# Performance work log

Measured on AMD Instinct MI355X. Metric: run time of the kernel, lower is better.

The kernel has to match this reference:

```python
import jax, jax.numpy as jnp
import numpy as np

N_NODES = 100000
N_EDGES = 1600000
N_GRAPHS = 512


def gcn_conv(x, W, b, src, dst, n_nodes):
    """GCNConv with self-loops: D^-1/2 (A+I) D^-1/2 X W + b."""
    h = x @ W  # [N, out]
    ones = jnp.ones((src.shape[0],), h.dtype)
    deg = jax.ops.segment_sum(ones, dst, num_segments=n_nodes) + 1.0  # +1 self-loop
    dinv = jax.lax.rsqrt(deg)
    norm = dinv[src] * dinv[dst]  # [E]
    agg = jax.ops.segment_sum(h[src] * norm[:, None], dst, num_segments=n_nodes)
    agg = agg + h * (1.0 / deg)[:, None]  # self-loop term: deg^-0.5 * deg^-0.5
    return agg + b


def setup_inputs() -> dict:
    key = jax.random.key(0)
    ks = jax.random.split(key, 12)
    x = jax.random.normal(ks[0], (N_NODES, 78), dtype=jnp.float32)
    edge_index = jax.random.randint(ks[1], (2, N_EDGES), 0, N_NODES, dtype=jnp.int64)
    batch = jnp.sort(jax.random.randint(ks[2], (N_NODES,), 0, N_GRAPHS, dtype=jnp.int64))
    def glorot(k, shape):
        lim = np.sqrt(6.0 / (shape[0] + shape[1])).astype(np.float32)
        return jax.random.uniform(k, shape, jnp.float32, -lim, lim)
    return {
        "x": x,
        "edge_index": edge_index,
        "batch": batch,
        "W1": glorot(ks[3], (78, 128)),
        "b1": jnp.zeros((128,), jnp.float32),
        "W2": glorot(ks[4], (128, 256)),
        "b2": jnp.zeros((256,), jnp.float32),
        "Wg1": glorot(ks[5], (256, 1024)),
        "bg1": jnp.zeros((1024,), jnp.float32),
        "Wg2": glorot(ks[6], (1024, 128)),
        "bg2": jnp.zeros((128,), jnp.float32),
    }


def reference(x, edge_index, batch, W1, b1, W2, b2, Wg1, bg1, Wg2, bg2):
    src, dst = edge_index[0], edge_index[1]
    n = x.shape[0]
    h = jax.nn.relu(gcn_conv(x, W1, b1, src, dst, n))   # [N,128]
    h = jax.nn.relu(gcn_conv(h, W2, b2, src, dst, n))   # [N,256]
    g = jax.ops.segment_max(h, batch, num_segments=N_GRAPHS)  # global max pool [G,256]
    g = jax.nn.relu(g @ Wg1 + bg1)   # [G,1024]; dropout is identity at eval
    g = g @ Wg2 + bg2                # [G,128]
    return g
```

## Files before the change

### kernel.cpp

```cpp
#include <hip/hip_runtime.h>
#include <hip/hip_bf16.h>


#define NN 100000
#define NE 1600000
#define NG 512
#define NBLK ((NN + 1023) / 1024)

typedef float v2f __attribute__((ext_vector_type(2)));


__global__ void k_zero_int(int* p, int n) {
    int i = blockIdx.x * blockDim.x + threadIdx.x;
    if (i < n) p[i] = 0;
}

__global__ void k_hist(const int* __restrict__ dst, int* cnt, int e) {
    int i = blockIdx.x * blockDim.x + threadIdx.x;
    if (i < e) atomicAdd(&cnt[dst[i]], 1);
}

__global__ void k_prep(const int* __restrict__ cnt, float* __restrict__ dinv,
                       float* __restrict__ gmax) {
    int i = blockIdx.x * blockDim.x + threadIdx.x;
    if (i < NN) dinv[i] = rsqrtf((float)cnt[i] + 1.0f);
    if (i < NG * 256) gmax[i] = 0.0f;
}

__global__ __launch_bounds__(256) void k_bsum(const int* __restrict__ cnt, int* __restrict__ bsum) {
    __shared__ int s[256];
    int b = blockIdx.x, t = threadIdx.x;
    int base = b * 1024 + t * 4;
    int v = 0;
#pragma unroll
    for (int j = 0; j < 4; j++) { int i = base + j; if (i < NN) v += cnt[i]; }
    s[t] = v; __syncthreads();
    for (int off = 128; off > 0; off >>= 1) {
        if (t < off) s[t] += s[t + off];
        __syncthreads();
    }
    if (t == 0) bsum[b] = s[0];
}

__global__ __launch_bounds__(128) void k_scan_bsum(int* bsum, int* row_ptr) {
    __shared__ int s[128];
    int t = threadIdx.x;
    int v = (t < NBLK) ? bsum[t] : 0;
    s[t] = v; __syncthreads();
    for (int off = 1; off < 128; off <<= 1) {
        int u = (t >= off) ? s[t - off] : 0;
        __syncthreads();
        s[t] += u;
        __syncthreads();
    }
    if (t < NBLK) bsum[t] = s[t] - v;
    if (t == 0) row_ptr[NN] = NE;
}

__global__ __launch_bounds__(256) void k_scan_blocks(const int* __restrict__ cnt,
    const int* __restrict__ bsum, int* __restrict__ row_ptr, int* __restrict__ cursor) {
    __shared__ int s[256];
    int b = blockIdx.x, t = threadIdx.x;
    int base = b * 1024 + t * 4;
    int v[4]; int sum = 0;
#pragma unroll
    for (int j = 0; j < 4; j++) { int i = base + j; v[j] = (i < NN) ? cnt[i] : 0; sum += v[j]; }
    s[t] = sum; __syncthreads();
    for (int off = 1; off < 256; off <<= 1) {
        int u = (t >= off) ? s[t - off] : 0;
        __syncthreads();
        s[t] += u;
        __syncthreads();
    }
    int excl = s[t] - sum + bsum[b];
#pragma unroll
    for (int j = 0; j < 4; j++) {
        int i = base + j;
        if (i < NN) { row_ptr[i] = excl; cursor[i] = excl; excl += v[j]; }
    }
}

__global__ void k_fillslots(const int* __restrict__ src, const int* __restrict__ dst,
    const float* __restrict__ dinv, int* cursor, int2* __restrict__ es, int e) {
    int i = blockIdx.x * blockDim.x + threadIdx.x;
    if (i >= e) return;
    int s = src[i], d = dst[i];
    int pos = atomicAdd(&cursor[d], 1);
    es[pos] = make_int2(s, __float_as_int(dinv[s] * dinv[d]));
}

__global__ __launch_bounds__(256) void k_fused1(const float* __restrict__ x,
    const int* __restrict__ rp, const int2* __restrict__ es,
    const float* __restrict__ dinv, const float* __restrict__ W,
    const float* __restrict__ bias, float* __restrict__ out) {
    __shared__ float As[4][8][80];
    int tid = threadIdx.x;
    int wv = tid >> 6, l = tid & 63;
    int task = __builtin_amdgcn_readfirstlane(blockIdx.x * 4 + wv);
    int n0 = task * 8;
    if (n0 >= NN) return;

    if (l < 39) {
        for (int pi = 0; pi < 4; pi++) {
            int nA = n0 + 2 * pi, nB = nA + 1;
            float diA = dinv[nA], swA = diA * diA;
            float diB = dinv[nB], swB = diB * diB;
            float2 aA = ((const float2*)(x + (size_t)nA * 78))[l];
            float2 aB = ((const float2*)(x + (size_t)nB * 78))[l];
            aA.x *= swA; aA.y *= swA;
            aB.x *= swB; aB.y *= swB;
            int eA = rp[nA], eA1 = rp[nA + 1];
            int eB = rp[nB], eB1 = rp[nB + 1];
            int cA = (eA1 - eA) >> 3, cB = (eB1 - eB) >> 3;
            while (cA > 0 || cB > 0) {
                bool dA = (cA > 0), dB = (cB > 0);
                int2 esA[8], esB[8];
                float2 vA[8], vB[8];
                if (dA) {
#pragma unroll
                    for (int j = 0; j < 8; j++) esA[j] = es[eA + j];
                }
                if (dB) {
#pragma unroll
                    for (int j = 0; j < 8; j++) esB[j] = es[eB + j];
                }
                if (dA) {
#pragma unroll
                    for (int j = 0; j < 8; j++)
                        vA[j] = ((const float2*)(x + (size_t)esA[j].x * 78))[l];
                }
                if (dB) {
#pragma unroll
                    for (int j = 0; j < 8; j++)
                        vB[j] = ((const float2*)(x + (size_t)esB[j].x * 78))[l];
                }
                if (dA) {
#pragma unroll
                    for (int j = 0; j < 8; j++) {
                        float w = __int_as_float(esA[j].y);
                        aA.x += vA[j].x * w; aA.y += vA[j].y * w;
                    }
                    eA += 8; cA--;
                }
                if (dB) {
#pragma unroll
                    for (int j = 0; j < 8; j++) {
                        float w = __int_as_float(esB[j].y);
                        aB.x += vB[j].x * w; aB.y += vB[j].y * w;
                    }
                    eB += 8; cB--;
                }
            }
            while (eA < eA1 && eB < eB1) {
                int2 pA = es[eA], pB = es[eB];
                float2 vA2 = ((const float2*)(x + (size_t)pA.x * 78))[l];
                float2 vB2 = ((const float2*)(x + (size_t)pB.x * 78))[l];
                float wA = __int_as_float(pA.y), wB = __int_as_float(pB.y);
                aA.x += vA2.x * wA; aA.y += vA2.y * wA;
                aB.x += vB2.x * wB; aB.y += vB2.y * wB;
                eA++; eB++;
            }
            for (; eA < eA1; eA++) {
                int2 p = es[eA];
                float w = __int_as_float(p.y);
                float2 v = ((const float2*)(x + (size_t)p.x * 78))[l];
                aA.x += v.x * w; aA.y += v.y * w;
            }
            for (; eB < eB1; eB++) {
                int2 p = es[eB];
                float w = __int_as_float(p.y);
                float2 v = ((const float2*)(x + (size_t)p.x * 78))[l];
                aB.x += v.x * w; aB.y += v.y * w;
            }
            *(float2*)&As[wv][2 * pi][2 * l] = aA;
            *(float2*)&As[wv][2 * pi + 1][2 * l] = aB;
        }
    }

    int f0 = l * 2;
    float2 acc[8];
#pragma unroll
    for (int i = 0; i < 8; i++) acc[i] = make_float2(0.f, 0.f);

    for (int k = 0; k < 76; k += 4) {
        float2 w0 = *(const float2*)&W[(k + 0) * 128 + f0];
        float2 w1 = *(const float2*)&W[(k + 1) * 128 + f0];
        float2 w2 = *(const float2*)&W[(k + 2) * 128 + f0];
        float2 w3 = *(const float2*)&W[(k + 3) * 128 + f0];
#pragma unroll
        for (int i = 0; i < 8; i++) {
            float4 a = *(const float4*)&As[wv][i][k];
            acc[i].x += a.x * w0.x + a.y * w1.x + a.z * w2.x + a.w * w3.x;
            acc[i].y += a.x * w0.y + a.y * w1.y + a.z * w2.y + a.w * w3.y;
        }
    }
    {
        float2 w0 = *(const float2*)&W[76 * 128 + f0];
        float2 w1 = *(const float2*)&W[77 * 128 + f0];
#pragma unroll
        for (int i = 0; i < 8; i++) {
            float2 a = *(const float2*)&As[wv][i][76];
            acc[i].x += a.x * w0.x + a.y * w1.x;
            acc[i].y += a.x * w0.y + a.y * w1.y;
        }
    }
    float2 bv = *(const float2*)&bias[f0];
#pragma unroll
    for (int i = 0; i < 8; i++) {
        float2 o;
        o.x = fmaxf(acc[i].x + bv.x, 0.f);
        o.y = fmaxf(acc[i].y + bv.y, 0.f);
        *(float2*)&out[(size_t)(n0 + i) * 128 + f0] = o;
    }
}

__global__ __launch_bounds__(256) void k_fused2(const float* __restrict__ h,
    const int* __restrict__ rp, const int2* __restrict__ es,
    const float* __restrict__ dinv, const float* __restrict__ W,
    const float* __restrict__ bias, const int* __restrict__ batch,
    unsigned* __restrict__ gmax) {
    __shared__ float As[4][8][128];
    int tid = threadIdx.x;
    int wv = tid >> 6, l = tid & 63;
    int task = __builtin_amdgcn_readfirstlane(blockIdx.x * 4 + wv);
    int n0 = task * 8;
    if (n0 >= NN) return;

    for (int pi = 0; pi < 4; pi++) {
        int nA = n0 + 2 * pi, nB = nA + 1;
        float diA = dinv[nA], swA = diA * diA;
        float diB = dinv[nB], swB = diB * diB;
        float2 aA = ((const float2*)(h + (size_t)nA * 128))[l];
        float2 aB = ((const float2*)(h + (size_t)nB * 128))[l];
        aA.x *= swA; aA.y *= swA;
        aB.x *= swB; aB.y *= swB;
        int eA = rp[nA], eA1 = rp[nA + 1];
        int eB = rp[nB], eB1 = rp[nB + 1];
        int cA = (eA1 - eA) >> 3, cB = (eB1 - eB) >> 3;
        while (cA > 0 || cB > 0) {
            bool dA = (cA > 0), dB = (cB > 0);
            int2 esA[8], esB[8];
            float2 vA[8], vB[8];
            if (dA) {
#pragma unroll
                for (int j = 0; j < 8; j++) esA[j] = es[eA + j];
            }
            if (dB) {
#pragma unroll
                for (int j = 0; j < 8; j++) esB[j] = es[eB + j];
            }
            if (dA) {
#pragma unroll
                for (int j = 0; j < 8; j++)
                    vA[j] = ((const float2*)(h + (size_t)esA[j].x * 128))[l];
            }
            if (dB) {
#pragma unroll
                for (int j = 0; j < 8; j++)
                    vB[j] = ((const float2*)(h + (size_t)esB[j].x * 128))[l];
            }
            if (dA) {
#pragma unroll
                for (int j = 0; j < 8; j++) {
                    float w = __int_as_float(esA[j].y);
                    aA.x += vA[j].x * w; aA.y += vA[j].y * w;
                }
                eA += 8; cA--;
            }
            if (dB) {
#pragma unroll
                for (int j = 0; j < 8; j++) {
                    float w = __int_as_float(esB[j].y);
                    aB.x += vB[j].x * w; aB.y += vB[j].y * w;
                }
                eB += 8; cB--;
            }
        }
        while (eA < eA1 && eB < eB1) {
            int2 pA = es[eA], pB = es[eB];
            float2 vA2 = ((const float2*)(h + (size_t)pA.x * 128))[l];
            float2 vB2 = ((const float2*)(h + (size_t)pB.x * 128))[l];
            float wA = __int_as_float(pA.y), wB = __int_as_float(pB.y);
            aA.x += vA2.x * wA; aA.y += vA2.y * wA;
            aB.x += vB2.x * wB; aB.y += vB2.y * wB;
            eA++; eB++;
        }
        for (; eA < eA1; eA++) {
            int2 p = es[eA];
            float w = __int_as_float(p.y);
            float2 v = ((const float2*)(h + (size_t)p.x * 128))[l];
            aA.x += v.x * w; aA.y += v.y * w;
        }
        for (; eB < eB1; eB++) {
            int2 p = es[eB];
            float w = __int_as_float(p.y);
            float2 v = ((const float2*)(h + (size_t)p.x * 128))[l];
            aB.x += v.x * w; aB.y += v.y * w;
        }
        *(float2*)&As[wv][2 * pi][2 * l] = aA;
        *(float2*)&As[wv][2 * pi + 1][2 * l] = aB;
    }

    int f0 = l * 4;
    v2f acc[8][2];
#pragma unroll
    for (int i = 0; i < 8; i++) { acc[i][0] = (v2f)(0.f); acc[i][1] = (v2f)(0.f); }

    for (int k = 0; k < 128; k += 4) {
        float4 w0 = *(const float4*)&W[(size_t)(k + 0) * 256 + f0];
        float4 w1 = *(const float4*)&W[(size_t)(k + 1) * 256 + f0];
        float4 w2 = *(const float4*)&W[(size_t)(k + 2) * 256 + f0];
        float4 w3 = *(const float4*)&W[(size_t)(k + 3) * 256 + f0];
        v2f w0a = {w0.x, w0.y}, w0b = {w0.z, w0.w};
        v2f w1a = {w1.x, w1.y}, w1b = {w1.z, w1.w};
        v2f w2a = {w2.x, w2.y}, w2b = {w2.z, w2.w};
        v2f w3a = {w3.x, w3.y}, w3b = {w3.z, w3.w};
#pragma unroll
        for (int i = 0; i < 8; i++) {
            float4 a = *(const float4*)&As[wv][i][k];
            v2f sx = {a.x, a.x}, sy = {a.y, a.y}, sz = {a.z, a.z}, sw = {a.w, a.w};
            acc[i][0] = __builtin_elementwise_fma(sx, w0a, acc[i][0]);
            acc[i][1] = __builtin_elementwise_fma(sx, w0b, acc[i][1]);
            acc[i][0] = __builtin_elementwise_fma(sy, w1a, acc[i][0]);
            acc[i][1] = __builtin_elementwise_fma(sy, w1b, acc[i][1]);
            acc[i][0] = __builtin_elementwise_fma(sz, w2a, acc[i][0]);
            acc[i][1] = __builtin_elementwise_fma(sz, w2b, acc[i][1]);
            acc[i][0] = __builtin_elementwise_fma(sw, w3a, acc[i][0]);
            acc[i][1] = __builtin_elementwise_fma(sw, w3b, acc[i][1]);
        }
    }

    float4 bv = *(const float4*)&bias[f0];
    int curg = -1;
    float4 m = make_float4(0.f, 0.f, 0.f, 0.f);
#pragma unroll
    for (int i = 0; i < 8; i++) {
        int g = batch[n0 + i];
        float4 v;
        v.x = fmaxf(acc[i][0].x + bv.x, 0.f); v.y = fmaxf(acc[i][0].y + bv.y, 0.f);
        v.z = fmaxf(acc[i][1].x + bv.z, 0.f); v.w = fmaxf(acc[i][1].y + bv.w, 0.f);
        if (g != curg) {
            if (curg >= 0) {
                unsigned* gp = &gmax[(size_t)curg * 256 + f0];
                atomicMax(&gp[0], __float_as_uint(m.x));
                atomicMax(&gp[1], __float_as_uint(m.y));
                atomicMax(&gp[2], __float_as_uint(m.z));
                atomicMax(&gp[3], __float_as_uint(m.w));
            }
            curg = g; m = v;
        } else {
            m.x = fmaxf(m.x, v.x); m.y = fmaxf(m.y, v.y);
            m.z = fmaxf(m.z, v.z); m.w = fmaxf(m.w, v.w);
        }
    }
    if (curg >= 0) {
        unsigned* gp = &gmax[(size_t)curg * 256 + f0];
        atomicMax(&gp[0], __float_as_uint(m.x));
        atomicMax(&gp[1], __float_as_uint(m.y));
        atomicMax(&gp[2], __float_as_uint(m.z));
        atomicMax(&gp[3], __float_as_uint(m.w));
    }
}


__global__ __launch_bounds__(256) void k_gemm3(const float* __restrict__ A,
    const float* __restrict__ W, const float* __restrict__ bias,
    float* __restrict__ out) {
    __shared__ float rs[256];
    int g = blockIdx.x, tid = threadIdx.x;
    rs[tid] = A[g * 256 + tid];
    __syncthreads();
    float acc[4] = {0.f, 0.f, 0.f, 0.f};
    for (int k = 0; k < 256; k++) {
        float a = rs[k];
#pragma unroll
        for (int j = 0; j < 4; j++) acc[j] += a * W[k * 1024 + tid + j * 256];
    }
#pragma unroll
    for (int j = 0; j < 4; j++) {
        int f = tid + j * 256;
        out[g * 1024 + f] = fmaxf(acc[j] + bias[f], 0.0f);
    }
}

__global__ __launch_bounds__(128) void k_gemm4(const float* __restrict__ A,
    const float* __restrict__ W, const float* __restrict__ bias,
    float* __restrict__ out) {
    __shared__ float rs[1024];
    int g = blockIdx.x, tid = threadIdx.x;
    for (int i = tid; i < 1024; i += 128) rs[i] = A[g * 1024 + i];
    __syncthreads();
    float acc = 0.0f;
    for (int k = 0; k < 1024; k++) acc += rs[k] * W[k * 128 + tid];
    out[g * 128 + tid] = acc + bias[tid];
}

extern "C" void kernel_launch(void* const* d_in, const int* in_sizes, int n_in,
                              void* d_out, int out_size, void* d_ws, size_t ws_size,
                              hipStream_t stream) {
    const float* x    = (const float*)d_in[0];
    const int*   ei   = (const int*)d_in[1];
    const int*   batch= (const int*)d_in[2];
    const float* W1   = (const float*)d_in[3];
    const float* b1   = (const float*)d_in[4];
    const float* W2   = (const float*)d_in[5];
    const float* b2   = (const float*)d_in[6];
    const float* Wg1  = (const float*)d_in[7];
    const float* bg1  = (const float*)d_in[8];
    const float* Wg2  = (const float*)d_in[9];
    const float* bg2  = (const float*)d_in[10];
    const int* src = ei;
    const int* dst = ei + NE;

    char* w8 = (char*)d_ws;
    int*   cnt     = (int*)w8;                 w8 += (size_t)NN * 4;
    int*   row_ptr = (int*)w8;                 w8 += (size_t)(NN + 4) * 4;
    int*   cursor  = (int*)w8;                 w8 += (size_t)NN * 4;
    int*   bsum    = (int*)w8;                 w8 += 128 * 4;
    int2*  es      = (int2*)w8;                w8 += (size_t)NE * 8;
    float* dinv    = (float*)w8;               w8 += (size_t)NN * 4;
    float* h1      = (float*)w8;               w8 += (size_t)NN * 128 * 4;
    unsigned* gmax = (unsigned*)w8;            w8 += (size_t)NG * 256 * 4;
    float* g1      = (float*)w8;               w8 += (size_t)NG * 1024 * 4;

    k_zero_int<<<(NN + 255) / 256, 256, 0, stream>>>(cnt, NN);
    k_hist<<<(NE + 255) / 256, 256, 0, stream>>>(dst, cnt, NE);
    k_prep<<<(NG * 256 + 255) / 256, 256, 0, stream>>>(cnt, dinv, (float*)gmax);
    k_bsum<<<NBLK, 256, 0, stream>>>(cnt, bsum);
    k_scan_bsum<<<1, 128, 0, stream>>>(bsum, row_ptr);
    k_scan_blocks<<<NBLK, 256, 0, stream>>>(cnt, bsum, row_ptr, cursor);
    k_fillslots<<<(NE + 255) / 256, 256, 0, stream>>>(src, dst, dinv, cursor, es, NE);

    k_fused1<<<NN / 32, 256, 0, stream>>>(x, row_ptr, es, dinv, W1, b1, h1);

    k_fused2<<<NN / 32, 256, 0, stream>>>(h1, row_ptr, es, dinv, W2, b2, batch, gmax);

    k_gemm3<<<NG, 256, 0, stream>>>((const float*)gmax, Wg1, bg1, g1);
    k_gemm4<<<NG, 128, 0, stream>>>(g1, Wg2, bg2, (float*)d_out);
}
```

Baseline: 587.5 us.

## Process two node tiles per wave, batch four graphs in head GEMMs, memset counts

Result: slower. 911.0 us (+55.1%).

```diff
diff --git a/kernel.cpp b/kernel.cpp
--- a/kernel.cpp
+++ b/kernel.cpp
@@ -9,11 +9,6 @@
 
 typedef float v2f __attribute__((ext_vector_type(2)));
 
-
-__global__ void k_zero_int(int* p, int n) {
-    int i = blockIdx.x * blockDim.x + threadIdx.x;
-    if (i < n) p[i] = 0;
-}
 
 __global__ void k_hist(const int* __restrict__ dst, int* cnt, int e) {
     int i = blockIdx.x * blockDim.x + threadIdx.x;
@@ -96,17 +91,166 @@
     __shared__ float As[4][8][80];
     int tid = threadIdx.x;
     int wv = tid >> 6, l = tid & 63;
-    int task = __builtin_amdgcn_readfirstlane(blockIdx.x * 4 + wv);
-    int n0 = task * 8;
-    if (n0 >= NN) return;
-
+    int w = __builtin_amdgcn_readfirstlane(blockIdx.x * 4 + wv);
+    if (w >= 6250) return;
+    int n0 = w * 16;
+
+    int f0 = l * 2;
+    float2 bv = *(const float2*)&bias[f0];
+
+    float2 init[8];
     if (l < 39) {
+#pragma unroll
+        for (int i = 0; i < 8; i++)
+            init[i] = ((const float2*)(x + (size_t)(n0 + i) * 78))[l];
+    }
+
+    for (int it = 0; it < 2; it++) {
+        int b0 = n0 + it * 8;
+        if (l < 39) {
+            for (int pi = 0; pi < 4; pi++) {
+                int nA = b0 + 2 * pi, nB = nA + 1;
+                float diA = dinv[nA], swA = diA * diA;
+                float diB = dinv[nB], swB = diB * diB;
+                float2 aA = init[2 * pi], aB = init[2 * pi + 1];
+                aA.x *= swA; aA.y *= swA;
+                aB.x *= swB; aB.y *= swB;
+                int eA = rp[nA], eA1 = rp[nA + 1];
+                int eB = rp[nB], eB1 = rp[nB + 1];
+                int cA = (eA1 - eA) >> 3, cB = (eB1 - eB) >> 3;
+                while (cA > 0 || cB > 0) {
+                    bool dA = (cA > 0), dB = (cB > 0);
+                    int2 esA[8], esB[8];
+                    float2 vA[8], vB[8];
+                    if (dA) {
+#pragma unroll
+                        for (int j = 0; j < 8; j++) esA[j] = es[eA + j];
+                    }
+                    if (dB) {
+#pragma unroll
+                        for (int j = 0; j < 8; j++) esB[j] = es[eB + j];
+                    }
+                    if (dA) {
+#pragma unroll
+                        for (int j = 0; j < 8; j++)
+                            vA[j] = ((const float2*)(x + (size_t)esA[j].x * 78))[l];
+                    }
+                    if (dB) {
+#pragma unroll
+                        for (int j = 0; j < 8; j++)
+                            vB[j] = ((const float2*)(x + (size_t)esB[j].x * 78))[l];
+                    }
+                    if (dA) {
+#pragma unroll
+                        for (int j = 0; j < 8; j++) {
+                            float ww = __int_as_float(esA[j].y);
+                            aA.x += vA[j].x * ww; aA.y += vA[j].y * ww;
+                        }
+                        eA += 8; cA--;
+                    }
+                    if (dB) {
+#pragma unroll
+                        for (int j = 0; j < 8; j++) {
+                            float ww = __int_as_float(esB[j].y);
+                            aB.x += vB[j].x * ww; aB.y += vB[j].y * ww;
+                        }
+                        eB += 8; cB--;
+                    }
+                }
+                while (eA < eA1 && eB < eB1) {
+                    int2 pA = es[eA], pB = es[eB];
+                    float2 vA2 = ((const float2*)(x + (size_t)pA.x * 78))[l];
+                    float2 vB2 = ((const float2*)(x + (size_t)pB.x * 78))[l];
+                    float wA = __int_as_float(pA.y), wB = __int_as_float(pB.y);
+                    aA.x += vA2.x * wA; aA.y += vA2.y * wA;
+                    aB.x += vB2.x * wB; aB.y += vB2.y * wB;
+                    eA++; eB++;
+                }
+                for (; eA < eA1; eA++) {
+                    int2 p = es[eA];
+                    float ww = __int_as_float(p.y);
+                    float2 v = ((const float2*)(x + (size_t)p.x * 78))[l];
+                    aA.x += v.x * ww; aA.y += v.y * ww;
+                }
+                for (; eB < eB1; eB++) {
+                    int2 p = es[eB];
+                    float ww = __int_as_float(p.y);
+                    float2 v = ((const float2*)(x + (size_t)p.x * 78))[l];
+                    aB.x += v.x * ww; aB.y += v.y * ww;
+                }
+                *(float2*)&As[wv][2 * pi][2 * l] = aA;
+                *(float2*)&As[wv][2 * pi + 1][2 * l] = aB;
+            }
+            if (it == 0) {
+#pragma unroll
+                for (int i = 0; i < 8; i++)
+                    init[i] = ((const float2*)(x + (size_t)(b0 + 8 + i) * 78))[l];
+            }
+        }
+
+        float2 acc[8];
+#pragma unroll
+        for (int i = 0; i < 8; i++) acc[i] = make_float2(0.f, 0.f);
+
+        for (int k = 0; k < 76; k += 4) {
+            float2 w0 = *(const float2*)&W[(k + 0) * 128 + f0];
+            float2 w1 = *(const float2*)&W[(k + 1) * 128 + f0];
+            float2 w2 = *(const float2*)&W[(k + 2) * 128 + f0];
+            float2 w3 = *(const float2*)&W[(k + 3) * 128 + f0];
+#pragma unroll
+            for (int i = 0; i < 8; i++) {
+                float4 a = *(const float4*)&As[wv][i][k];
+                acc[i].x += a.x * w0.x + a.y * w1.x + a.z * w2.x + a.w * w3.x;
+                acc[i].y += a.x * w0.y + a.y * w1.y + a.z * w2.y + a.w * w3.y;
+            }
+        }
+        {
+            float2 w0 = *(const float2*)&W[76 * 128 + f0];
+            float2 w1 = *(const float2*)&W[77 * 128 + f0];
+#pragma unroll
+            for (int i = 0; i < 8; i++) {
+                float2 a = *(const float2*)&As[wv][i][76];
+                acc[i].x += a.x * w0.x + a.y * w1.x;
+                acc[i].y += a.x * w0.y + a.y * w1.y;
+            }
+        }
+#pragma unroll
+        for (int i = 0; i < 8; i++) {
+            float2 o;
+            o.x = fmaxf(acc[i].x + bv.x, 0.f);
+            o.y = fmaxf(acc[i].y + bv.y, 0.f);
+            *(float2*)&out[(size_t)(b0 + i) * 128 + f0] = o;
+        }
+    }
+}
+
+__global__ __launch_bounds__(256) void k_fused2(const float* __restrict__ h,
+    const int* __restrict__ rp, const int2* __restrict__ es,
+    const float* __restrict__ dinv, const float* __restrict__ W,
+    const float* __restrict__ bias, const int* __restrict__ batch,
+    unsigned* __restrict__ gmax) {
+    __shared__ float As[4][8][128];
+    int tid = threadIdx.x;
+    int wv = tid >> 6, l = tid & 63;
+    int w = __builtin_amdgcn_readfirstlane(blockIdx.x * 4 + wv);
+    if (w >= 6250) return;
+    int n0 = w * 16;
+
+    int f0 = l * 4;
+    float4 bv = *(const float4*)&bias[f0];
+
+    float2 init[8];
+#pragma unroll
+    for (int i = 0; i < 8; i++)
+        init[i] = ((const float2*)(h + (size_t)(n0 + i) * 128))[l];
+
+    for (int it = 0; it < 2; it++) {
+        int b0 = n0 + it * 8;
         for (int pi = 0; pi < 4; pi++) {
-            int nA = n0 + 2 * pi, nB = nA + 1;
+            int nA = b0 + 2 * pi, nB = nA + 1;
             float diA = dinv[nA], swA = diA * diA;
             float diB = dinv[nB], swB = diB * diB;
-            float2 aA = ((const float2*)(x + (size_t)nA * 78))[l];
-            float2 aB = ((const float2*)(x + (size_t)nB * 78))[l];
+            float2 aA = init[2 * pi], aB = init[2 * pi + 1];
             aA.x *= swA; aA.y *= swA;
             aB.x *= swB; aB.y *= swB;
             int eA = rp[nA], eA1 = rp[nA + 1];
@@ -127,34 +271,34 @@
                 if (dA) {
 #pragma unroll
                     for (int j = 0; j < 8; j++)
-                        vA[j] = ((const float2*)(x + (size_t)esA[j].x * 78))[l];
+                        vA[j] = ((const float2*)(h + (size_t)esA[j].x * 128))[l];
                 }
                 if (dB) {
 #pragma unroll
                     for (int j = 0; j < 8; j++)
-                        vB[j] = ((const float2*)(x + (size_t)esB[j].x * 78))[l];
+                        vB[j] = ((const float2*)(h + (size_t)esB[j].x * 128))[l];
                 }
                 if (dA) {
 #pragma unroll
                     for (int j = 0; j < 8; j++) {
-                        float w = __int_as_float(esA[j].y);
-                        aA.x += vA[j].x * w; aA.y += vA[j].y * w;
+                        float ww = __int_as_float(esA[j].y);
+                        aA.x += vA[j].x * ww; aA.y += vA[j].y * ww;
                     }
                     eA += 8; cA--;
                 }
                 if (dB) {
 #pragma unroll
                     for (int j = 0; j < 8; j++) {
-                        float w = __int_as_float(esB[j].y);
-                        aB.x += vB[j].x * w; aB.y += vB[j].y * w;
+                        float ww = __int_as_float(esB[j].y);
+                        aB.x += vB[j].x * ww; aB.y += vB[j].y * ww;
                     }
                     eB += 8; cB--;
                 }
             }
             while (eA < eA1 && eB < eB1) {
                 int2 pA = es[eA], pB = es[eB];
-                float2 vA2 = ((const float2*)(x + (size_t)pA.x * 78))[l];
-                float2 vB2 = ((const float2*)(x + (size_t)pB.x * 78))[l];
+                float2 vA2 = ((const float2*)(h + (size_t)pA.x * 128))[l];
+                float2 vB2 = ((const float2*)(h + (size_t)pB.x * 128))[l];
                 float wA = __int_as_float(pA.y), wB = __int_as_float(pB.y);
                 aA.x += vA2.x * wA; aA.y += vA2.y * wA;
                 aB.x += vB2.x * wB; aB.y += vB2.y * wB;
@@ -162,203 +306,82 @@
             }
             for (; eA < eA1; eA++) {
                 int2 p = es[eA];
-                float w = __int_as_float(p.y);
-                float2 v = ((const float2*)(x + (size_t)p.x * 78))[l];
-                aA.x += v.x * w; aA.y += v.y * w;
+                float ww = __int_as_float(p.y);
+                float2 v = ((const float2*)(h + (size_t)p.x * 128))[l];
+                aA.x += v.x * ww; aA.y += v.y * ww;
             }
             for (; eB < eB1; eB++) {
                 int2 p = es[eB];
-                float w = __int_as_float(p.y);
-                float2 v = ((const float2*)(x + (size_t)p.x * 78))[l];
-                aB.x += v.x * w; aB.y += v.y * w;
+                float ww = __int_as_float(p.y);
+                float2 v = ((const float2*)(h + (size_t)p.x * 128))[l];
+                aB.x += v.x * ww; aB.y += v.y * ww;
             }
             *(float2*)&As[wv][2 * pi][2 * l] = aA;
             *(float2*)&As[wv][2 * pi + 1][2 * l] = aB;
         }
-    }
-
-    int f0 = l * 2;
-    float2 acc[8];
-#pragma unroll
-    for (int i = 0; i < 8; i++) acc[i] = make_float2(0.f, 0.f);
-
-    for (int k = 0; k < 76; k += 4) {
-        float2 w0 = *(const float2*)&W[(k + 0) * 128 + f0];
-        float2 w1 = *(const float2*)&W[(k + 1) * 128 + f0];
-        float2 w2 = *(const float2*)&W[(k + 2) * 128 + f0];
-        float2 w3 = *(const float2*)&W[(k + 3) * 128 + f0];
+        if (it == 0) {
+#pragma unroll
+            for (int i = 0; i < 8; i++)
+                init[i] = ((const float2*)(h + (size_t)(b0 + 8 + i) * 128))[l];
+        }
+
+        v2f acc[8][2];
+#pragma unroll
+        for (int i = 0; i < 8; i++) { acc[i][0] = (v2f)(0.f); acc[i][1] = (v2f)(0.f); }
+
+        for (int k = 0; k < 128; k += 4) {
+            float4 w0 = *(const float4*)&W[(size_t)(k + 0) * 256 + f0];
+            float4 w1 = *(const float4*)&W[(size_t)(k + 1) * 256 + f0];
+            float4 w2 = *(const float4*)&W[(size_t)(k + 2) * 256 + f0];
+            float4 w3 = *(const float4*)&W[(size_t)(k + 3) * 256 + f0];
+            v2f w0a = {w0.x, w0.y}, w0b = {w0.z, w0.w};
+            v2f w1a = {w1.x, w1.y}, w1b = {w1.z, w1.w};
+            v2f w2a = {w2.x, w2.y}, w2b = {w2.z, w2.w};
+            v2f w3a = {w3.x, w3.y}, w3b = {w3.z, w3.w};
+#pragma unroll
+            for (int i = 0; i < 8; i++) {
+                float4 a = *(const float4*)&As[wv][i][k];
+                v2f sx = {a.x, a.x}, sy = {a.y, a.y}, sz = {a.z, a.z}, sw = {a.w, a.w};
+                acc[i][0] = __builtin_elementwise_fma(sx, w0a, acc[i][0]);
+                acc[i][1] = __builtin_elementwise_fma(sx, w0b, acc[i][1]);
+                acc[i][0] = __builtin_elementwise_fma(sy, w1a, acc[i][0]);
+                acc[i][1] = __builtin_elementwise_fma(sy, w1b, acc[i][1]);
+                acc[i][0] = __builtin_elementwise_fma(sz, w2a, acc[i][0]);
+                acc[i][1] = __builtin_elementwise_fma(sz, w2b, acc[i][1]);
+                acc[i][0] = __builtin_elementwise_fma(sw, w3a, acc[i][0]);
+                acc[i][1] = __builtin_elementwise_fma(sw, w3b, acc[i][1]);
+            }
+        }
+
+        int curg = -1;
+        float4 m = make_float4(0.f, 0.f, 0.f, 0.f);
 #pragma unroll
         for (int i = 0; i < 8; i++) {
-            float4 a = *(const float4*)&As[wv][i][k];
-            acc[i].x += a.x * w0.x + a.y * w1.x + a.z * w2.x + a.w * w3.x;
-            acc[i].y += a.x * w0.y + a.y * w1.y + a.z * w2.y + a.w * w3.y;
-        }
-    }
-    {
-        float2 w0 = *(const float2*)&W[76 * 128 + f0];
-        float2 w1 = *(const float2*)&W[77 * 128 + f0];
-#pragma unroll
-        for (int i = 0; i < 8; i++) {
-            float2 a = *(const float2*)&As[wv][i][76];
-            acc[i].x += a.x * w0.x + a.y * w1.x;
-            acc[i].y += a.x * w0.y + a.y * w1.y;
-        }
-    }
-    float2 bv = *(const float2*)&bias[f0];
-#pragma unroll
-    for (int i = 0; i < 8; i++) {
-        float2 o;
-        o.x = fmaxf(acc[i].x + bv.x, 0.f);
-        o.y = fmaxf(acc[i].y + bv.y, 0.f);
-        *(float2*)&out[(size_t)(n0 + i) * 128 + f0] = o;
-    }
-}
-
-__global__ __launch_bounds__(256) void k_fused2(const float* __restrict__ h,
-    const int* __restrict__ rp, const int2* __restrict__ es,
-    const float* __restrict__ dinv, const float* __restrict__ W,
-    const float* __restrict__ bias, const int* __restrict__ batch,
-    unsigned* __restrict__ gmax) {
-    __shared__ float As[4][8][128];
-    int tid = threadIdx.x;
-    int wv = tid >> 6, l = tid & 63;
-    int task = __builtin_amdgcn_readfirstlane(blockIdx.x * 4 + wv);
-    int n0 = task * 8;
-    if (n0 >= NN) return;
-
-    for (int pi = 0; pi < 4; pi++) {
-        int nA = n0 + 2 * pi, nB = nA + 1;
-        float diA = dinv[nA], swA = diA * diA;
-        float diB = dinv[nB], swB = diB * diB;
-        float2 aA = ((const float2*)(h + (size_t)nA * 128))[l];
-        float2 aB = ((const float2*)(h + (size_t)nB * 128))[l];
-        aA.x *= swA; aA.y *= swA;
-        aB.x *= swB; aB.y *= swB;
-        int eA = rp[nA], eA1 = rp[nA + 1];
-        int eB = rp[nB], eB1 = rp[nB + 1];
-        int cA = (eA1 - eA) >> 3, cB = (eB1 - eB) >> 3;
-        while (cA > 0 || cB > 0) {
-            bool dA = (cA > 0), dB = (cB > 0);
-            int2 esA[8], esB[8];
-            float2 vA[8], vB[8];
-            if (dA) {
-#pragma unroll
-                for (int j = 0; j < 8; j++) esA[j] = es[eA + j];
-            }
-            if (dB) {
-#pragma unroll
-                for (int j = 0; j < 8; j++) esB[j] = es[eB + j];
-            }
-            if (dA) {
-#pragma unroll
-                for (int j = 0; j < 8; j++)
-                    vA[j] = ((const float2*)(h + (size_t)esA[j].x * 128))[l];
-            }
-            if (dB) {
-#pragma unroll
-                for (int j = 0; j < 8; j++)
-                    vB[j] = ((const float2*)(h + (size_t)esB[j].x * 128))[l];
-            }
-            if (dA) {
-#pragma unroll
-                for (int j = 0; j < 8; j++) {
-                    float w = __int_as_float(esA[j].y);
-                    aA.x += vA[j].x * w; aA.y += vA[j].y * w;
-                }
-                eA += 8; cA--;
-            }
-            if (dB) {
-#pragma unroll
-                for (int j = 0; j < 8; j++) {
-                    float w = __int_as_float(esB[j].y);
-                    aB.x += vB[j].x * w; aB.y += vB[j].y * w;
-                }
-                eB += 8; cB--;
-            }
-        }
-        while (eA < eA1 && eB < eB1) {
-            int2 pA = es[eA], pB = es[eB];
-            float2 vA2 = ((const float2*)(h + (size_t)pA.x * 128))[l];
-            float2 vB2 = ((const float2*)(h + (size_t)pB.x * 128))[l];
-            float wA = __int_as_float(pA.y), wB = __int_as_float(pB.y);
-            aA.x += vA2.x * wA; aA.y += vA2.y * wA;
-            aB.x += vB2.x * wB; aB.y += vB2.y * wB;
-            eA++; eB++;
-        }
-        for (; eA < eA1; eA++) {
-            int2 p = es[eA];
-            float w = __int_as_float(p.y);
-            float2 v = ((const float2*)(h + (size_t)p.x * 128))[l];
-            aA.x += v.x * w; aA.y += v.y * w;
-        }
-        for (; eB < eB1; eB++) {
-            int2 p = es[eB];
-            float w = __int_as_float(p.y);
-            float2 v = ((const float2*)(h + (size_t)p.x * 128))[l];
-            aB.x += v.x * w; aB.y += v.y * w;
-        }
-        *(float2*)&As[wv][2 * pi][2 * l] = aA;
-        *(float2*)&As[wv][2 * pi + 1][2 * l] = aB;
-    }
-
-    int f0 = l * 4;
-    v2f acc[8][2];
-#pragma unroll
-    for (int i = 0; i < 8; i++) { acc[i][0] = (v2f)(0.f); acc[i][1] = (v2f)(0.f); }
-
-    for (int k = 0; k < 128; k += 4) {
-        float4 w0 = *(const float4*)&W[(size_t)(k + 0) * 256 + f0];
-        float4 w1 = *(const float4*)&W[(size_t)(k + 1) * 256 + f0];
-        float4 w2 = *(const float4*)&W[(size_t)(k + 2) * 256 + f0];
-        float4 w3 = *(const float4*)&W[(size_t)(k + 3) * 256 + f0];
-        v2f w0a = {w0.x, w0.y}, w0b = {w0.z, w0.w};
-        v2f w1a = {w1.x, w1.y}, w1b = {w1.z, w1.w};
-        v2f w2a = {w2.x, w2.y}, w2b = {w2.z, w2.w};
-        v2f w3a = {w3.x, w3.y}, w3b = {w3.z, w3.w};
-#pragma unroll
-        for (int i = 0; i < 8; i++) {
-            float4 a = *(const float4*)&As[wv][i][k];
-            v2f sx = {a.x, a.x}, sy = {a.y, a.y}, sz = {a.z, a.z}, sw = {a.w, a.w};
-            acc[i][0] = __builtin_elementwise_fma(sx, w0a, acc[i][0]);
-            acc[i][1] = __builtin_elementwise_fma(sx, w0b, acc[i][1]);
-            acc[i][0] = __builtin_elementwise_fma(sy, w1a, acc[i][0]);
-            acc[i][1] = __builtin_elementwise_fma(sy, w1b, acc[i][1]);
-            acc[i][0] = __builtin_elementwise_fma(sz, w2a, acc[i][0]);
-            acc[i][1] = __builtin_elementwise_fma(sz, w2b, acc[i][1]);
-            acc[i][0] = __builtin_elementwise_fma(sw, w3a, acc[i][0]);
-            acc[i][1] = __builtin_elementwise_fma(sw, w3b, acc[i][1]);
-        }
-    }
-
-    float4 bv = *(const float4*)&bias[f0];
-    int curg = -1;
-    float4 m = make_float4(0.f, 0.f, 0.f, 0.f);
-#pragma unroll
-    for (int i = 0; i < 8; i++) {
-        int g = batch[n0 + i];
-        float4 v;
-        v.x = fmaxf(acc[i][0].x + bv.x, 0.f); v.y = fmaxf(acc[i][0].y + bv.y, 0.f);
-        v.z = fmaxf(acc[i][1].x + bv.z, 0.f); v.w = fmaxf(acc[i][1].y + bv.w, 0.f);
-        if (g != curg) {
-            if (curg >= 0) {
-                unsigned* gp = &gmax[(size_t)curg * 256 + f0];
-                atomicMax(&gp[0], __float_as_uint(m.x));
-                atomicMax(&gp[1], __float_as_uint(m.y));
-                atomicMax(&gp[2], __float_as_uint(m.z));
-                atomicMax(&gp[3], __float_as_uint(m.w));
-            }
-            curg = g; m = v;
-        } else {
-            m.x = fmaxf(m.x, v.x); m.y = fmaxf(m.y, v.y);
-            m.z = fmaxf(m.z, v.z); m.w = fmaxf(m.w, v.w);
-        }
-    }
-    if (curg >= 0) {
-        unsigned* gp = &gmax[(size_t)curg * 256 + f0];
-        atomicMax(&gp[0], __float_as_uint(m.x));
-        atomicMax(&gp[1], __float_as_uint(m.y));
-        atomicMax(&gp[2], __float_as_uint(m.z));
-        atomicMax(&gp[3], __float_as_uint(m.w));
+            int g = batch[b0 + i];
+            float4 v;
+            v.x = fmaxf(acc[i][0].x + bv.x, 0.f); v.y = fmaxf(acc[i][0].y + bv.y, 0.f);
+            v.z = fmaxf(acc[i][1].x + bv.z, 0.f); v.w = fmaxf(acc[i][1].y + bv.w, 0.f);
+            if (g != curg) {
+                if (curg >= 0) {
+                    unsigned* gp = &gmax[(size_t)curg * 256 + f0];
+                    atomicMax(&gp[0], __float_as_uint(m.x));
+                    atomicMax(&gp[1], __float_as_uint(m.y));
+                    atomicMax(&gp[2], __float_as_uint(m.z));
+                    atomicMax(&gp[3], __float_as_uint(m.w));
+                }
+                curg = g; m = v;
+            } else {
+                m.x = fmaxf(m.x, v.x); m.y = fmaxf(m.y, v.y);
+                m.z = fmaxf(m.z, v.z); m.w = fmaxf(m.w, v.w);
+            }
+        }
+        if (curg >= 0) {
+            unsigned* gp = &gmax[(size_t)curg * 256 + f0];
+            atomicMax(&gp[0], __float_as_uint(m.x));
+            atomicMax(&gp[1], __float_as_uint(m.y));
+            atomicMax(&gp[2], __float_as_uint(m.z));
+            atomicMax(&gp[3], __float_as_uint(m.w));
+        }
     }
 }
 
@@ -366,33 +389,53 @@
 __global__ __launch_bounds__(256) void k_gemm3(const float* __restrict__ A,
     const float* __restrict__ W, const float* __restrict__ bias,
     float* __restrict__ out) {
-    __shared__ float rs[256];
-    int g = blockIdx.x, tid = threadIdx.x;
-    rs[tid] = A[g * 256 + tid];
+    __shared__ float rs[4][256];
+    int b = blockIdx.x, tid = threadIdx.x;
+#pragma unroll
+    for (int g = 0; g < 4; g++) rs[g][tid] = A[(b * 4 + g) * 256 + tid];
     __syncthreads();
-    float acc[4] = {0.f, 0.f, 0.f, 0.f};
+    float acc[4][4];
+#pragma unroll
+    for (int g = 0; g < 4; g++)
+#pragma unroll
+        for (int j = 0; j < 4; j++) acc[g][j] = 0.f;
     for (int k = 0; k < 256; k++) {
-        float a = rs[k];
-#pragma unroll
-        for (int j = 0; j < 4; j++) acc[j] += a * W[k * 1024 + tid + j * 256];
-    }
-#pragma unroll
-    for (int j = 0; j < 4; j++) {
-        int f = tid + j * 256;
-        out[g * 1024 + f] = fmaxf(acc[j] + bias[f], 0.0f);
-    }
+        float w0 = W[k * 1024 + tid];
+        float w1 = W[k * 1024 + tid + 256];
+        float w2 = W[k * 1024 + tid + 512];
+        float w3 = W[k * 1024 + tid + 768];
+#pragma unroll
+        for (int g = 0; g < 4; g++) {
+            float a = rs[g][k];
+            acc[g][0] += a * w0; acc[g][1] += a * w1;
+            acc[g][2] += a * w2; acc[g][3] += a * w3;
+        }
+    }
+#pragma unroll
+    for (int g = 0; g < 4; g++)
+#pragma unroll
+        for (int j = 0; j < 4; j++) {
+            int f = tid + j * 256;
+            out[(b * 4 + g) * 1024 + f] = fmaxf(acc[g][j] + bias[f], 0.0f);
+        }
 }
 
 __global__ __launch_bounds__(128) void k_gemm4(const float* __restrict__ A,
     const float* __restrict__ W, const float* __restrict__ bias,
     float* __restrict__ out) {
-    __shared__ float rs[1024];
-    int g = blockIdx.x, tid = threadIdx.x;
-    for (int i = tid; i < 1024; i += 128) rs[i] = A[g * 1024 + i];
+    __shared__ float rs[4][1024];
+    int b = blockIdx.x, tid = threadIdx.x;
+    for (int i = tid; i < 4096; i += 128) rs[i >> 10][i & 1023] = A[b * 4096 + i];
     __syncthreads();
-    float acc = 0.0f;
-    for (int k = 0; k < 1024; k++) acc += rs[k] * W[k * 128 + tid];
-    out[g * 128 + tid] = acc + bias[tid];
+    float acc[4] = {0.f, 0.f, 0.f, 0.f};
+    for (int k = 0; k < 1024; k++) {
+        float wv = W[k * 128 + tid];
+#pragma unroll
+        for (int g = 0; g < 4; g++) acc[g] += rs[g][k] * wv;
+    }
+#pragma unroll
+    for (int g = 0; g < 4; g++)
+        out[(b * 4 + g) * 128 + tid] = acc[g] + bias[tid];
 }
 
 extern "C" void kernel_launch(void* const* d_in, const int* in_sizes, int n_in,
@@ -423,7 +466,7 @@
     unsigned* gmax = (unsigned*)w8;            w8 += (size_t)NG * 256 * 4;
     float* g1      = (float*)w8;               w8 += (size_t)NG * 1024 * 4;
 
-    k_zero_int<<<(NN + 255) / 256, 256, 0, stream>>>(cnt, NN);
+    hipMemsetAsync(cnt, 0, (size_t)NN * 4, stream);
     k_hist<<<(NE + 255) / 256, 256, 0, stream>>>(dst, cnt, NE);
     k_prep<<<(NG * 256 + 255) / 256, 256, 0, stream>>>(cnt, dinv, (float*)gmax);
     k_bsum<<<NBLK, 256, 0, stream>>>(cnt, bsum);
@@ -431,10 +474,10 @@
     k_scan_blocks<<<NBLK, 256, 0, stream>>>(cnt, bsum, row_ptr, cursor);
     k_fillslots<<<(NE + 255) / 256, 256, 0, stream>>>(src, dst, dinv, cursor, es, NE);
 
-    k_fused1<<<NN / 32, 256, 0, stream>>>(x, row_ptr, es, dinv, W1, b1, h1);
-
-    k_fused2<<<NN / 32, 256, 0, stream>>>(h1, row_ptr, es, dinv, W2, b2, batch, gmax);
-
-    k_gemm3<<<NG, 256, 0, stream>>>((const float*)gmax, Wg1, bg1, g1);
-    k_gemm4<<<NG, 128, 0, stream>>>(g1, Wg2, bg2, (float*)d_out);
-}
+    k_fused1<<<1563, 256, 0, stream>>>(x, row_ptr, es, dinv, W1, b1, h1);
+
+    k_fused2<<<1563, 256, 0, stream>>>(h1, row_ptr, es, dinv, W2, b2, batch, gmax);
+
+    k_gemm3<<<NG / 4, 256, 0, stream>>>((const float*)gmax, Wg1, bg1, g1);
+    k_gemm4<<<NG / 4, 128, 0, stream>>>(g1, Wg2, bg2, (float*)d_out);
+}
```

## Store layer-1 activations in fp16, batch graphs in head GEMMs, use memset

Applied to the files above, without the earlier changes.

Result: no change. 580.9 us (-1.1%).

```diff
diff --git a/kernel.cpp b/kernel.cpp
--- a/kernel.cpp
+++ b/kernel.cpp
@@ -1,5 +1,5 @@
 #include <hip/hip_runtime.h>
-#include <hip/hip_bf16.h>
+#include <hip/hip_fp16.h>
 
 
 #define NN 100000
@@ -9,11 +9,6 @@
 
 typedef float v2f __attribute__((ext_vector_type(2)));
 
-
-__global__ void k_zero_int(int* p, int n) {
-    int i = blockIdx.x * blockDim.x + threadIdx.x;
-    if (i < n) p[i] = 0;
-}
 
 __global__ void k_hist(const int* __restrict__ dst, int* cnt, int e) {
     int i = blockIdx.x * blockDim.x + threadIdx.x;
@@ -92,7 +87,7 @@
 __global__ __launch_bounds__(256) void k_fused1(const float* __restrict__ x,
     const int* __restrict__ rp, const int2* __restrict__ es,
     const float* __restrict__ dinv, const float* __restrict__ W,
-    const float* __restrict__ bias, float* __restrict__ out) {
+    const float* __restrict__ bias, __half* __restrict__ out) {
     __shared__ float As[4][8][80];
     int tid = threadIdx.x;
     int wv = tid >> 6, l = tid & 63;
@@ -207,14 +202,13 @@
     float2 bv = *(const float2*)&bias[f0];
 #pragma unroll
     for (int i = 0; i < 8; i++) {
-        float2 o;
-        o.x = fmaxf(acc[i].x + bv.x, 0.f);
-        o.y = fmaxf(acc[i].y + bv.y, 0.f);
-        *(float2*)&out[(size_t)(n0 + i) * 128 + f0] = o;
-    }
-}
-
-__global__ __launch_bounds__(256) void k_fused2(const float* __restrict__ h,
+        float ox = fmaxf(acc[i].x + bv.x, 0.f);
+        float oy = fmaxf(acc[i].y + bv.y, 0.f);
+        *(__half2*)&out[(size_t)(n0 + i) * 128 + f0] = __floats2half2_rn(ox, oy);
+    }
+}
+
+__global__ __launch_bounds__(256) void k_fused2(const __half* __restrict__ h,
     const int* __restrict__ rp, const int2* __restrict__ es,
     const float* __restrict__ dinv, const float* __restrict__ W,
     const float* __restrict__ bias, const int* __restrict__ batch,
@@ -230,8 +224,8 @@
         int nA = n0 + 2 * pi, nB = nA + 1;
         float diA = dinv[nA], swA = diA * diA;
         float diB = dinv[nB], swB = diB * diB;
-        float2 aA = ((const float2*)(h + (size_t)nA * 128))[l];
-        float2 aB = ((const float2*)(h + (size_t)nB * 128))[l];
+        float2 aA = __half22float2(((const __half2*)(h + (size_t)nA * 128))[l]);
+        float2 aB = __half22float2(((const __half2*)(h + (size_t)nB * 128))[l]);
         aA.x *= swA; aA.y *= swA;
         aB.x *= swB; aB.y *= swB;
         int eA = rp[nA], eA1 = rp[nA + 1];
@@ -240,7 +234,7 @@
         while (cA > 0 || cB > 0) {
             bool dA = (cA > 0), dB = (cB > 0);
             int2 esA[8], esB[8];
-            float2 vA[8], vB[8];
+            __half2 vA[8], vB[8];
             if (dA) {
 #pragma unroll
                 for (int j = 0; j < 8; j++) esA[j] = es[eA + j];
@@ -252,18 +246,19 @@
             if (dA) {
 #pragma unroll
                 for (int j = 0; j < 8; j++)
-                    vA[j] = ((const float2*)(h + (size_t)esA[j].x * 128))[l];
+                    vA[j] = ((const __half2*)(h + (size_t)esA[j].x * 128))[l];
             }
             if (dB) {
 #pragma unroll
                 for (int j = 0; j < 8; j++)
-                    vB[j] = ((const float2*)(h + (size_t)esB[j].x * 128))[l];
+                    vB[j] = ((const __half2*)(h + (size_t)esB[j].x * 128))[l];
             }
             if (dA) {
 #pragma unroll
                 for (int j = 0; j < 8; j++) {
                     float w = __int_as_float(esA[j].y);
-                    aA.x += vA[j].x * w; aA.y += vA[j].y * w;
+                    float2 v = __half22float2(vA[j]);
+                    aA.x += v.x * w; aA.y += v.y * w;
                 }
                 eA += 8; cA--;
             }
@@ -271,15 +266,16 @@
 #pragma unroll
                 for (int j = 0; j < 8; j++) {
                     float w = __int_as_float(esB[j].y);
-                    aB.x += vB[j].x * w; aB.y += vB[j].y * w;
+                    float2 v = __half22float2(vB[j]);
+                    aB.x += v.x * w; aB.y += v.y * w;
                 }
                 eB += 8; cB--;
             }
         }
         while (eA < eA1 && eB < eB1) {
             int2 pA = es[eA], pB = es[eB];
-            float2 vA2 = ((const float2*)(h + (size_t)pA.x * 128))[l];
-            float2 vB2 = ((const float2*)(h + (size_t)pB.x * 128))[l];
+            float2 vA2 = __half22float2(((const __half2*)(h + (size_t)pA.x * 128))[l]);
+            float2 vB2 = __half22float2(((const __half2*)(h + (size_t)pB.x * 128))[l]);
             float wA = __int_as_float(pA.y), wB = __int_as_float(pB.y);
             aA.x += vA2.x * wA; aA.y += vA2.y * wA;
             aB.x += vB2.x * wB; aB.y += vB2.y * wB;
@@ -288,13 +284,13 @@
         for (; eA < eA1; eA++) {
             int2 p = es[eA];
             float w = __int_as_float(p.y);
-            float2 v = ((const float2*)(h + (size_t)p.x * 128))[l];
+            float2 v = __half22float2(((const __half2*)(h + (size_t)p.x * 128))[l]);
             aA.x += v.x * w; aA.y += v.y * w;
         }
         for (; eB < eB1; eB++) {
             int2 p = es[eB];
             float w = __int_as_float(p.y);
-            float2 v = ((const float2*)(h + (size_t)p.x * 128))[l];
+            float2 v = __half22float2(((const __half2*)(h + (size_t)p.x * 128))[l]);
             aB.x += v.x * w; aB.y += v.y * w;
         }
         *(float2*)&As[wv][2 * pi][2 * l] = aA;
@@ -366,33 +362,53 @@
 __global__ __launch_bounds__(256) void k_gemm3(const float* __restrict__ A,
     const float* __restrict__ W, const float* __restrict__ bias,
     float* __restrict__ out) {
-    __shared__ float rs[256];
-    int g = blockIdx.x, tid = threadIdx.x;
-    rs[tid] = A[g * 256 + tid];
+    __shared__ float rs[4][256];
+    int b = blockIdx.x, tid = threadIdx.x;
+#pragma unroll
+    for (int g = 0; g < 4; g++) rs[g][tid] = A[(b * 4 + g) * 256 + tid];
     __syncthreads();
-    float acc[4] = {0.f, 0.f, 0.f, 0.f};
+    float acc[4][4];
+#pragma unroll
+    for (int g = 0; g < 4; g++)
+#pragma unroll
+        for (int j = 0; j < 4; j++) acc[g][j] = 0.f;
     for (int k = 0; k < 256; k++) {
-        float a = rs[k];
-#pragma unroll
-        for (int j = 0; j < 4; j++) acc[j] += a * W[k * 1024 + tid + j * 256];
-    }
-#pragma unroll
-    for (int j = 0; j < 4; j++) {
-        int f = tid + j * 256;
-        out[g * 1024 + f] = fmaxf(acc[j] + bias[f], 0.0f);
-    }
+        float w0 = W[k * 1024 + tid];
+        float w1 = W[k * 1024 + tid + 256];
+        float w2 = W[k * 1024 + tid + 512];
+        float w3 = W[k * 1024 + tid + 768];
+#pragma unroll
+        for (int g = 0; g < 4; g++) {
+            float a = rs[g][k];
+            acc[g][0] += a * w0; acc[g][1] += a * w1;
+            acc[g][2] += a * w2; acc[g][3] += a * w3;
+        }
+    }
+#pragma unroll
+    for (int g = 0; g < 4; g++)
+#pragma unroll
+        for (int j = 0; j < 4; j++) {
+            int f = tid + j * 256;
+            out[(b * 4 + g) * 1024 + f] = fmaxf(acc[g][j] + bias[f], 0.0f);
+        }
 }
 
 __global__ __launch_bounds__(128) void k_gemm4(const float* __restrict__ A,
     const float* __restrict__ W, const float* __restrict__ bias,
     float* __restrict__ out) {
-    __shared__ float rs[1024];
-    int g = blockIdx.x, tid = threadIdx.x;
-    for (int i = tid; i < 1024; i += 128) rs[i] = A[g * 1024 + i];
+    __shared__ float rs[4][1024];
+    int b = blockIdx.x, tid = threadIdx.x;
+    for (int i = tid; i < 4096; i += 128) rs[i >> 10][i & 1023] = A[b * 4096 + i];
     __syncthreads();
-    float acc = 0.0f;
-    for (int k = 0; k < 1024; k++) acc += rs[k] * W[k * 128 + tid];
-    out[g * 128 + tid] = acc + bias[tid];
+    float acc[4] = {0.f, 0.f, 0.f, 0.f};
+    for (int k = 0; k < 1024; k++) {
+        float wv = W[k * 128 + tid];
+#pragma unroll
+        for (int g = 0; g < 4; g++) acc[g] += rs[g][k] * wv;
+    }
+#pragma unroll
+    for (int g = 0; g < 4; g++)
+        out[(b * 4 + g) * 128 + tid] = acc[g] + bias[tid];
 }
 
 extern "C" void kernel_launch(void* const* d_in, const int* in_sizes, int n_in,
@@ -419,11 +435,11 @@
     int*   bsum    = (int*)w8;                 w8 += 128 * 4;
     int2*  es      = (int2*)w8;                w8 += (size_t)NE * 8;
     float* dinv    = (float*)w8;               w8 += (size_t)NN * 4;
-    float* h1      = (float*)w8;               w8 += (size_t)NN * 128 * 4;
+    __half* h1     = (__half*)w8;              w8 += (size_t)NN * 128 * 2;
     unsigned* gmax = (unsigned*)w8;            w8 += (size_t)NG * 256 * 4;
     float* g1      = (float*)w8;               w8 += (size_t)NG * 1024 * 4;
 
-    k_zero_int<<<(NN + 255) / 256, 256, 0, stream>>>(cnt, NN);
+    hipMemsetAsync(cnt, 0, (size_t)NN * 4, stream);
     k_hist<<<(NE + 255) / 256, 256, 0, stream>>>(dst, cnt, NE);
     k_prep<<<(NG * 256 + 255) / 256, 256, 0, stream>>>(cnt, dinv, (float*)gmax);
     k_bsum<<<NBLK, 256, 0, stream>>>(cnt, bsum);
@@ -435,6 +451,6 @@
 
     k_fused2<<<NN / 32, 256, 0, stream>>>(h1, row_ptr, es, dinv, W2, b2, batch, gmax);
 
-    k_gemm3<<<NG, 256, 0, stream>>>((const float*)gmax, Wg1, bg1, g1);
-    k_gemm4<<<NG, 128, 0, stream>>>(g1, Wg2, bg2, (float*)d_out);
-}
+    k_gemm3<<<NG / 4, 256, 0, stream>>>((const float*)gmax, Wg1, bg1, g1);
+    k_gemm4<<<NG / 4, 128, 0, stream>>>(g1, Wg2, bg2, (float*)d_out);
+}
```
